# Kernel tuning notes

Hardware: AMD Instinct MI355X
Metric: run time of the kernel (lower is better)

## Reference

```python
import jax, jax.numpy as jnp
import numpy as np

B, S, T, C, HS = 32, 8, 512, 128, 128


def setup_inputs() -> dict:
    key = jax.random.key(0)
    k1, k2, k3, k4, k5 = jax.random.split(key, 5)
    x = jax.random.normal(k1, (B, T, C), dtype=jnp.float32)
    adjacent = jax.random.uniform(k2, (B, S, T, T), dtype=jnp.float32)
    scale = 1.0 / np.sqrt(C)
    Wq = jax.random.normal(k3, (C, HS), dtype=jnp.float32) * scale
    Wk = jax.random.normal(k4, (C, HS), dtype=jnp.float32) * scale
    Wv = jax.random.normal(k5, (C, HS), dtype=jnp.float32) * scale
    return {"x": x, "adjacent": adjacent, "Wq": Wq, "Wk": Wk, "Wv": Wv}


def reference(x, adjacent, Wq, Wk, Wv):
    # x: [B,T,C], adjacent: [B,S,T,T]
    Cdim = x.shape[-1]
    q = x @ Wq            # [B,T,HS]
    k = x @ Wk            # [B,T,HS]
    v = x @ Wv            # [B,T,HS]
    # scaled scores (note: original scales by C^-0.5, not head_size^-0.5)
    wei = jnp.einsum('btd,bud->btu', q, k) * (Cdim ** -0.5)  # [B,T,T]
    # multiplicative adjacency mask, broadcast over S
    wei = wei[:, None, :, :] * adjacent                       # [B,S,T,T]
    wei = jax.nn.softmax(wei, axis=-1)
    # dropout p=0.0 -> identity
    out = jnp.einsum('bstu,bud->bstd', wei, v)                # [B,S,T,HS]
    return out
```

## Files before the change

### kernel.cpp

```cpp
#include <hip/hip_runtime.h>
#include <hip/hip_bf16.h>
#include <stdint.h>

#define NB 32
#define NS 8
#define NT 512
#define NC 128
#define NH 128

typedef __bf16 bf16_t;
typedef bf16_t bf16x8 __attribute__((ext_vector_type(8)));
typedef bf16_t bf16x4 __attribute__((ext_vector_type(4)));
typedef float  f32x4  __attribute__((ext_vector_type(4)));

__global__ __launch_bounds__(256) void k_split(const float* __restrict__ in,
                                               bf16_t* __restrict__ hi,
                                               bf16_t* __restrict__ lo, int n4) {
  int i = blockIdx.x * 256 + threadIdx.x;
  if (i >= n4) return;
  f32x4 x = ((const f32x4*)in)[i];
  bf16x4 h, l;
#pragma unroll
  for (int j = 0; j < 4; j++) {
    bf16_t hb = (bf16_t)x[j];
    h[j] = hb;
    l[j] = (bf16_t)(x[j] - (float)hb);
  }
  ((bf16x4*)hi)[i] = h;
  ((bf16x4*)lo)[i] = l;
}

__global__ void k_prep_w(const float* __restrict__ Wq, const float* __restrict__ Wk,
                         const float* __restrict__ Wv, bf16_t* __restrict__ Wth,
                         bf16_t* __restrict__ Wtl) {
  int w = blockIdx.x >> 7;
  int h = blockIdx.x & 127;
  int c = threadIdx.x;
  const float* W = (w == 0) ? Wq : (w == 1) ? Wk : Wv;
  float x = W[c * NH + h];
  bf16_t hb = (bf16_t)x;
  int o = (w * 128 + h) * 128 + c;
  Wth[o] = hb;
  Wtl[o] = (bf16_t)(x - (float)hb);
}

__global__ __launch_bounds__(256) void k_qkv(const bf16_t* __restrict__ xh,
                                             const bf16_t* __restrict__ xl,
                                             const bf16_t* __restrict__ Wth,
                                             const bf16_t* __restrict__ Wtl,
                                             bf16_t* __restrict__ qh,
                                             bf16_t* __restrict__ ql,
                                             bf16_t* __restrict__ kh,
                                             bf16_t* __restrict__ kl,
                                             bf16_t* __restrict__ vt) {
  int mat = blockIdx.y;
  int t0 = blockIdx.x * 64;
  int lane = threadIdx.x & 63;
  int wave = threadIdx.x >> 6;
  int l15 = lane & 15;
  int kq = (lane >> 4) * 8;
  int row = t0 + wave * 16 + l15;
  const bf16_t* Wh = Wth + mat * NC * NH;
  const bf16_t* Wl = Wtl + mat * NC * NH;

  f32x4 zero = {0.f, 0.f, 0.f, 0.f};
  f32x4 acc[8];
#pragma unroll
  for (int i = 0; i < 8; i++) acc[i] = zero;

#pragma unroll
  for (int k0 = 0; k0 < NC; k0 += 32) {
    bf16x8 ah = *(const bf16x8*)(xh + (size_t)row * NC + k0 + kq);
    bf16x8 al = *(const bf16x8*)(xl + (size_t)row * NC + k0 + kq);
#pragma unroll
    for (int nt = 0; nt < 8; nt++) {
      bf16x8 bh = *(const bf16x8*)(Wh + (nt * 16 + l15) * NC + k0 + kq);
      bf16x8 bl = *(const bf16x8*)(Wl + (nt * 16 + l15) * NC + k0 + kq);
      acc[nt] = __builtin_amdgcn_mfma_f32_16x16x32_bf16(ah, bh, acc[nt], 0, 0, 0);
      acc[nt] = __builtin_amdgcn_mfma_f32_16x16x32_bf16(ah, bl, acc[nt], 0, 0, 0);
      acc[nt] = __builtin_amdgcn_mfma_f32_16x16x32_bf16(al, bh, acc[nt], 0, 0, 0);
    }
  }

  int trow = t0 + wave * 16 + (lane >> 4) * 4;
  if (mat < 2) {
    bf16_t* dh = (mat == 0) ? qh : kh;
    bf16_t* dl = (mat == 0) ? ql : kl;
#pragma unroll
    for (int nt = 0; nt < 8; nt++) {
      int h = nt * 16 + l15;
#pragma unroll
      for (int r = 0; r < 4; r++) {
        float v = acc[nt][r];
        bf16_t hb = (bf16_t)v;
        dh[(size_t)(trow + r) * NH + h] = hb;
        dl[(size_t)(trow + r) * NH + h] = (bf16_t)(v - (float)hb);
      }
    }
  } else {
    int b = trow >> 9;
    int tl = trow & 511;
#pragma unroll
    for (int nt = 0; nt < 8; nt++) {
      int h = nt * 16 + l15;
      bf16x4 pk;
#pragma unroll
      for (int r = 0; r < 4; r++) pk[r] = (bf16_t)acc[nt][r];
      *(bf16x4*)(vt + ((size_t)b * NH + h) * NT + tl) = pk;
    }
  }
}

__global__ __launch_bounds__(256) void k_scores(const bf16_t* __restrict__ qh,
                                                const bf16_t* __restrict__ ql,
                                                const bf16_t* __restrict__ kh,
                                                const bf16_t* __restrict__ kl,
                                                float* __restrict__ wei) {
  int b = blockIdx.y;
  int mt = blockIdx.x >> 3;
  int ut = blockIdx.x & 7;
  int lane = threadIdx.x & 63;
  int wave = threadIdx.x >> 6;
  int l15 = lane & 15;
  int kq = (lane >> 4) * 8;
  int m0 = mt * 64 + wave * 16;
  int u0 = ut * 64;
  const float scale = 0.08838834764831845f;

  f32x4 zero = {0.f, 0.f, 0.f, 0.f};
  f32x4 acc[4];
#pragma unroll
  for (int i = 0; i < 4; i++) acc[i] = zero;

  size_t qbase = ((size_t)b * NT + m0 + l15) * NH;
  size_t kbase = ((size_t)b * NT + u0 + l15) * NH;

#pragma unroll
  for (int k0 = 0; k0 < NH; k0 += 32) {
    bf16x8 ah = *(const bf16x8*)(qh + qbase + k0 + kq);
    bf16x8 al = *(const bf16x8*)(ql + qbase + k0 + kq);
#pragma unroll
    for (int nt = 0; nt < 4; nt++) {
      bf16x8 bh = *(const bf16x8*)(kh + kbase + (size_t)nt * 16 * NH + k0 + kq);
      bf16x8 bl = *(const bf16x8*)(kl + kbase + (size_t)nt * 16 * NH + k0 + kq);
      acc[nt] = __builtin_amdgcn_mfma_f32_16x16x32_bf16(ah, bh, acc[nt], 0, 0, 0);
      acc[nt] = __builtin_amdgcn_mfma_f32_16x16x32_bf16(ah, bl, acc[nt], 0, 0, 0);
      acc[nt] = __builtin_amdgcn_mfma_f32_16x16x32_bf16(al, bh, acc[nt], 0, 0, 0);
    }
  }

  int t = m0 + (lane >> 4) * 4;
#pragma unroll
  for (int nt = 0; nt < 4; nt++) {
    int u = u0 + nt * 16 + l15;
#pragma unroll
    for (int r = 0; r < 4; r++)
      wei[((size_t)b * NT + t + r) * NT + u] = acc[nt][r] * scale;
  }
}

#define PLD 520

__global__ __launch_bounds__(256) void k_attn(const float* __restrict__ wei,
                                              const float* __restrict__ adj,
                                              const bf16_t* __restrict__ vt,
                                              float* __restrict__ out) {
  __shared__ bf16_t p[32 * PLD];
  int t0 = blockIdx.x * 32;
  int s = blockIdx.y;
  int b = blockIdx.z;
  int lane = threadIdx.x & 63;
  int wave = threadIdx.x >> 6;

#pragma unroll
  for (int rr = 0; rr < 8; rr++) {
    int r = wave * 8 + rr;
    const float* wrow = wei + ((size_t)b * NT + t0 + r) * NT;
    const float* arow = adj + (((size_t)b * NS + s) * NT + t0 + r) * NT;
    f32x4 w0 = ((const f32x4*)wrow)[lane];
    f32x4 w1 = ((const f32x4*)wrow)[64 + lane];
    f32x4 a0 = ((const f32x4*)arow)[lane];
    f32x4 a1 = ((const f32x4*)arow)[64 + lane];
    bf16x4 e0, e1;
#pragma unroll
    for (int j = 0; j < 4; j++) e0[j] = (bf16_t)__expf(w0[j] * a0[j]);
#pragma unroll
    for (int j = 0; j < 4; j++) e1[j] = (bf16_t)__expf(w1[j] * a1[j]);
    *(bf16x4*)&p[r * PLD + lane * 4] = e0;
    *(bf16x4*)&p[r * PLD + 256 + lane * 4] = e1;
  }
  __syncthreads();

  int l15 = lane & 15;
  int kq = (lane >> 4) * 8;
  int m0 = (wave & 1) * 16;
  int h0 = (wave >> 1) * 64;
  f32x4 zero = {0.f, 0.f, 0.f, 0.f};
  f32x4 acc[4];
#pragma unroll
  for (int i = 0; i < 4; i++) acc[i] = zero;
  f32x4 accl = zero;
  bf16x8 ones;
#pragma unroll
  for (int j = 0; j < 8; j++) ones[j] = (bf16_t)1.0f;
  const bf16_t* vb = vt + (size_t)b * NH * NT;

#pragma unroll 4
  for (int k0 = 0; k0 < NT; k0 += 32) {
    bf16x8 a = *(const bf16x8*)&p[(m0 + l15) * PLD + k0 + kq];
    accl = __builtin_amdgcn_mfma_f32_16x16x32_bf16(a, ones, accl, 0, 0, 0);
#pragma unroll
    for (int nt = 0; nt < 4; nt++) {
      bf16x8 bfr = *(const bf16x8*)(vb + (size_t)(h0 + nt * 16 + l15) * NT + k0 + kq);
      acc[nt] = __builtin_amdgcn_mfma_f32_16x16x32_bf16(a, bfr, acc[nt], 0, 0, 0);
    }
  }

  int tl = m0 + (lane >> 4) * 4;
  float linv[4];
#pragma unroll
  for (int r = 0; r < 4; r++) linv[r] = 1.0f / accl[r];
  float* obase = out + (((size_t)b * NS + s) * NT + t0) * NH;
#pragma unroll
  for (int nt = 0; nt < 4; nt++) {
    int h = h0 + nt * 16 + l15;
#pragma unroll
    for (int r = 0; r < 4; r++)
      obase[(size_t)(tl + r) * NH + h] = acc[nt][r] * linv[r];
  }
}

extern "C" void kernel_launch(void* const* d_in, const int* in_sizes, int n_in,
                              void* d_out, int out_size, void* d_ws, size_t ws_size,
                              hipStream_t stream) {
  const float* x = (const float*)d_in[0];
  const float* adj = (const float*)d_in[1];
  const float* Wq = (const float*)d_in[2];
  const float* Wk = (const float*)d_in[3];
  const float* Wv = (const float*)d_in[4];
  float* out = (float*)d_out;

  const size_t BTC = (size_t)NB * NT * NC;

  char* base = (char*)d_ws;
  bf16_t* xh = (bf16_t*)base;  base += BTC * 2;
  bf16_t* xl = (bf16_t*)base;  base += BTC * 2;
  bf16_t* Wth = (bf16_t*)base; base += (size_t)3 * NC * NH * 2;
  bf16_t* Wtl = (bf16_t*)base; base += (size_t)3 * NC * NH * 2;
  bf16_t* qh = (bf16_t*)base;  base += BTC * 2;
  bf16_t* ql = (bf16_t*)base;  base += BTC * 2;
  bf16_t* kh = (bf16_t*)base;  base += BTC * 2;
  bf16_t* kl = (bf16_t*)base;  base += BTC * 2;
  bf16_t* vt = (bf16_t*)base;  base += BTC * 2;
  float* wei = (float*)base;   base += (size_t)NB * NT * NT * 4;
  (void)in_sizes; (void)n_in; (void)out_size; (void)ws_size;

  k_split<<<(int)(BTC / 4 / 256), 256, 0, stream>>>(x, xh, xl, (int)(BTC / 4));
  k_prep_w<<<384, 128, 0, stream>>>(Wq, Wk, Wv, Wth, Wtl);
  k_qkv<<<dim3((int)(NB * NT / 64), 3), 256, 0, stream>>>(xh, xl, Wth, Wtl,
                                                          qh, ql, kh, kl, vt);
  k_scores<<<dim3(64, NB), 256, 0, stream>>>(qh, ql, kh, kl, wei);
  k_attn<<<dim3(NT / 32, NS, NB), 256, 0, stream>>>(wei, adj, vt, out);
}
```

Before: 535.3 us.

## Loop over S inside attention block with double-buffered P and adj prefetch

The attention kernel now handles a 16-row tile for all 8 S slices inside one block. The wei rows are loaded once per block and reused across S instead of being reloaded per slice. The adj rows for the next slice are prefetched into registers while the current slice's MFMA loop runs, and a double-buffered shared P tile lets compute overlap with writing the next exponentials. The trade-off is a smaller grid (1024 blocks) with a serial S loop, 16-row MFMA tiles that reuse V less per load, and higher register pressure under the launch_bounds(256,4) hint.

```diff
diff --git a/kernel.cpp b/kernel.cpp
--- a/kernel.cpp
+++ b/kernel.cpp
@@ -161,72 +161,92 @@
 
 #define PLD 520
 
-__global__ __launch_bounds__(256) void k_attn(const float* __restrict__ wei,
-                                              const float* __restrict__ adj,
-                                              const bf16_t* __restrict__ vt,
-                                              float* __restrict__ out) {
-  __shared__ bf16_t p[32 * PLD];
-  int t0 = blockIdx.x * 32;
-  int s = blockIdx.y;
-  int b = blockIdx.z;
+__global__ __launch_bounds__(256, 4) void k_attn(const float* __restrict__ wei,
+                                                 const float* __restrict__ adj,
+                                                 const bf16_t* __restrict__ vt,
+                                                 float* __restrict__ out) {
+  __shared__ bf16_t p[2][16 * PLD];
+  int t0 = blockIdx.x * 16;
+  int b = blockIdx.y;
   int lane = threadIdx.x & 63;
   int wave = threadIdx.x >> 6;
-
-#pragma unroll
-  for (int rr = 0; rr < 8; rr++) {
-    int r = wave * 8 + rr;
-    const float* wrow = wei + ((size_t)b * NT + t0 + r) * NT;
-    const float* arow = adj + (((size_t)b * NS + s) * NT + t0 + r) * NT;
-    f32x4 w0 = ((const f32x4*)wrow)[lane];
-    f32x4 w1 = ((const f32x4*)wrow)[64 + lane];
-    f32x4 a0 = ((const f32x4*)arow)[lane];
-    f32x4 a1 = ((const f32x4*)arow)[64 + lane];
-    bf16x4 e0, e1;
-#pragma unroll
-    for (int j = 0; j < 4; j++) e0[j] = (bf16_t)__expf(w0[j] * a0[j]);
-#pragma unroll
-    for (int j = 0; j < 4; j++) e1[j] = (bf16_t)__expf(w1[j] * a1[j]);
-    *(bf16x4*)&p[r * PLD + lane * 4] = e0;
-    *(bf16x4*)&p[r * PLD + 256 + lane * 4] = e1;
-  }
-  __syncthreads();
-
   int l15 = lane & 15;
   int kq = (lane >> 4) * 8;
-  int m0 = (wave & 1) * 16;
-  int h0 = (wave >> 1) * 64;
-  f32x4 zero = {0.f, 0.f, 0.f, 0.f};
-  f32x4 acc[4];
-#pragma unroll
-  for (int i = 0; i < 4; i++) acc[i] = zero;
-  f32x4 accl = zero;
+  int h0 = wave * 32;
+
+  f32x4 wf0[4], wf1[4];
+#pragma unroll
+  for (int rr = 0; rr < 4; rr++) {
+    const float* wrow = wei + ((size_t)b * NT + t0 + wave * 4 + rr) * NT;
+    wf0[rr] = ((const f32x4*)wrow)[lane];
+    wf1[rr] = ((const f32x4*)wrow)[64 + lane];
+  }
+
+  const bf16_t* vb = vt + (size_t)b * NH * NT;
   bf16x8 ones;
 #pragma unroll
   for (int j = 0; j < 8; j++) ones[j] = (bf16_t)1.0f;
-  const bf16_t* vb = vt + (size_t)b * NH * NT;
-
+
+  f32x4 a0[4], a1[4];
+#pragma unroll
+  for (int rr = 0; rr < 4; rr++) {
+    const float* arow = adj + ((size_t)b * NS * NT + t0 + wave * 4 + rr) * NT;
+    a0[rr] = ((const f32x4*)arow)[lane];
+    a1[rr] = ((const f32x4*)arow)[64 + lane];
+  }
+
+  for (int s = 0; s < NS; s++) {
+    bf16_t* pb = &p[s & 1][0];
+#pragma unroll
+    for (int rr = 0; rr < 4; rr++) {
+      int r = wave * 4 + rr;
+      bf16x4 e0, e1;
+#pragma unroll
+      for (int j = 0; j < 4; j++) e0[j] = (bf16_t)__expf(wf0[rr][j] * a0[rr][j]);
+#pragma unroll
+      for (int j = 0; j < 4; j++) e1[j] = (bf16_t)__expf(wf1[rr][j] * a1[rr][j]);
+      *(bf16x4*)&pb[r * PLD + lane * 4] = e0;
+      *(bf16x4*)&pb[r * PLD + 256 + lane * 4] = e1;
+    }
+    __syncthreads();
+
+    if (s + 1 < NS) {
+#pragma unroll
+      for (int rr = 0; rr < 4; rr++) {
+        const float* arow =
+            adj + (((size_t)b * NS + s + 1) * NT + t0 + wave * 4 + rr) * NT;
+        a0[rr] = ((const f32x4*)arow)[lane];
+        a1[rr] = ((const f32x4*)arow)[64 + lane];
+      }
+    }
+
+    f32x4 zero = {0.f, 0.f, 0.f, 0.f};
+    f32x4 acc[2] = {zero, zero};
+    f32x4 accl = zero;
 #pragma unroll 4
-  for (int k0 = 0; k0 < NT; k0 += 32) {
-    bf16x8 a = *(const bf16x8*)&p[(m0 + l15) * PLD + k0 + kq];
-    accl = __builtin_amdgcn_mfma_f32_16x16x32_bf16(a, ones, accl, 0, 0, 0);
-#pragma unroll
-    for (int nt = 0; nt < 4; nt++) {
-      bf16x8 bfr = *(const bf16x8*)(vb + (size_t)(h0 + nt * 16 + l15) * NT + k0 + kq);
-      acc[nt] = __builtin_amdgcn_mfma_f32_16x16x32_bf16(a, bfr, acc[nt], 0, 0, 0);
-    }
-  }
-
-  int tl = m0 + (lane >> 4) * 4;
-  float linv[4];
-#pragma unroll
-  for (int r = 0; r < 4; r++) linv[r] = 1.0f / accl[r];
-  float* obase = out + (((size_t)b * NS + s) * NT + t0) * NH;
-#pragma unroll
-  for (int nt = 0; nt < 4; nt++) {
-    int h = h0 + nt * 16 + l15;
-#pragma unroll
-    for (int r = 0; r < 4; r++)
-      obase[(size_t)(tl + r) * NH + h] = acc[nt][r] * linv[r];
+    for (int k0 = 0; k0 < NT; k0 += 32) {
+      bf16x8 afr = *(const bf16x8*)&pb[l15 * PLD + k0 + kq];
+      accl = __builtin_amdgcn_mfma_f32_16x16x32_bf16(afr, ones, accl, 0, 0, 0);
+#pragma unroll
+      for (int nt = 0; nt < 2; nt++) {
+        bf16x8 bfr =
+            *(const bf16x8*)(vb + (size_t)(h0 + nt * 16 + l15) * NT + k0 + kq);
+        acc[nt] = __builtin_amdgcn_mfma_f32_16x16x32_bf16(afr, bfr, acc[nt], 0, 0, 0);
+      }
+    }
+
+    int tl = (lane >> 4) * 4;
+    float linv[4];
+#pragma unroll
+    for (int r = 0; r < 4; r++) linv[r] = 1.0f / accl[r];
+    float* obase = out + (((size_t)b * NS + s) * NT + t0) * NH;
+#pragma unroll
+    for (int nt = 0; nt < 2; nt++) {
+      int h = h0 + nt * 16 + l15;
+#pragma unroll
+      for (int r = 0; r < 4; r++)
+        obase[(size_t)(tl + r) * NH + h] = acc[nt][r] * linv[r];
+    }
   }
 }
 
@@ -260,5 +280,5 @@
   k_qkv<<<dim3((int)(NB * NT / 64), 3), 256, 0, stream>>>(xh, xl, Wth, Wtl,
                                                           qh, ql, kh, kl, vt);
   k_scores<<<dim3(64, NB), 256, 0, stream>>>(qh, ql, kh, kl, wei);
-  k_attn<<<dim3(NT / 32, NS, NB), 256, 0, stream>>>(wei, adj, vt, out);
-}
+  k_attn<<<dim3(NT / 16, NB), 256, 0, stream>>>(wei, adj, vt, out);
+}
```

After: 534.2 us. About the same (-0.2%).

## Fuse score computation into attention kernel and fold scale into Wq

Applied to the files above, without the earlier changes.

Removes the separate scores kernel and the fp32 wei buffer in global memory. Each 512-thread block computes its 16-row score tile once with split-bf16 MFMA, then loops over all 8 S slices, applying the adjacency mask, exp and the PV product with a double-buffered LDS tile. The C^-0.5 scale is folded into Wq during weight prep. This saves writing and re-reading wei eight times, at the cost of smaller per-block tiles, adjacency loads of one float per lane, and serial S iterations inside each block.

```diff
diff --git a/kernel.cpp b/kernel.cpp
--- a/kernel.cpp
+++ b/kernel.cpp
@@ -38,6 +38,7 @@
   int c = threadIdx.x;
   const float* W = (w == 0) ? Wq : (w == 1) ? Wk : Wv;
   float x = W[c * NH + h];
+  if (w == 0) x *= 0.08838834764831845f;
   bf16_t hb = (bf16_t)x;
   int o = (w * 128 + h) * 128 + c;
   Wth[o] = hb;
@@ -111,122 +112,83 @@
   }
 }
 
-__global__ __launch_bounds__(256) void k_scores(const bf16_t* __restrict__ qh,
-                                                const bf16_t* __restrict__ ql,
-                                                const bf16_t* __restrict__ kh,
-                                                const bf16_t* __restrict__ kl,
-                                                float* __restrict__ wei) {
+#define PLD 520
+
+__global__ __launch_bounds__(512, 8) void k_attn(const bf16_t* __restrict__ qh,
+                                                 const bf16_t* __restrict__ ql,
+                                                 const bf16_t* __restrict__ kh,
+                                                 const bf16_t* __restrict__ kl,
+                                                 const float* __restrict__ adj,
+                                                 const bf16_t* __restrict__ vt,
+                                                 float* __restrict__ out) {
+  __shared__ bf16_t p[2][16 * PLD];
+  int t0 = blockIdx.x * 16;
   int b = blockIdx.y;
-  int mt = blockIdx.x >> 3;
-  int ut = blockIdx.x & 7;
   int lane = threadIdx.x & 63;
   int wave = threadIdx.x >> 6;
   int l15 = lane & 15;
-  int kq = (lane >> 4) * 8;
-  int m0 = mt * 64 + wave * 16;
-  int u0 = ut * 64;
-  const float scale = 0.08838834764831845f;
+  int q4 = lane >> 4;
+  int kq = q4 * 8;
+  int u0 = wave * 64;
+  int h0 = wave * 16;
 
   f32x4 zero = {0.f, 0.f, 0.f, 0.f};
-  f32x4 acc[4];
-#pragma unroll
-  for (int i = 0; i < 4; i++) acc[i] = zero;
-
-  size_t qbase = ((size_t)b * NT + m0 + l15) * NH;
-  size_t kbase = ((size_t)b * NT + u0 + l15) * NH;
-
-#pragma unroll
-  for (int k0 = 0; k0 < NH; k0 += 32) {
-    bf16x8 ah = *(const bf16x8*)(qh + qbase + k0 + kq);
-    bf16x8 al = *(const bf16x8*)(ql + qbase + k0 + kq);
+  f32x4 wacc[4];
+#pragma unroll
+  for (int i = 0; i < 4; i++) wacc[i] = zero;
+  {
+    size_t qb = ((size_t)b * NT + t0 + l15) * NH;
+    size_t kb = ((size_t)b * NT + u0 + l15) * NH;
+#pragma unroll
+    for (int k0 = 0; k0 < NH; k0 += 32) {
+      bf16x8 ah = *(const bf16x8*)(qh + qb + k0 + kq);
+      bf16x8 al = *(const bf16x8*)(ql + qb + k0 + kq);
+#pragma unroll
+      for (int nt = 0; nt < 4; nt++) {
+        bf16x8 bh = *(const bf16x8*)(kh + kb + (size_t)nt * 16 * NH + k0 + kq);
+        bf16x8 bl = *(const bf16x8*)(kl + kb + (size_t)nt * 16 * NH + k0 + kq);
+        wacc[nt] = __builtin_amdgcn_mfma_f32_16x16x32_bf16(ah, bh, wacc[nt], 0, 0, 0);
+        wacc[nt] = __builtin_amdgcn_mfma_f32_16x16x32_bf16(ah, bl, wacc[nt], 0, 0, 0);
+        wacc[nt] = __builtin_amdgcn_mfma_f32_16x16x32_bf16(al, bh, wacc[nt], 0, 0, 0);
+      }
+    }
+  }
+
+  const bf16_t* vb = vt + (size_t)b * NH * NT;
+  bf16x8 ones;
+#pragma unroll
+  for (int j = 0; j < 8; j++) ones[j] = (bf16_t)1.0f;
+
+  for (int s = 0; s < NS; s++) {
+    bf16_t* pb = &p[s & 1][0];
+    const float* abase =
+        adj + (((size_t)b * NS + s) * NT + t0 + q4 * 4) * NT + u0 + l15;
 #pragma unroll
     for (int nt = 0; nt < 4; nt++) {
-      bf16x8 bh = *(const bf16x8*)(kh + kbase + (size_t)nt * 16 * NH + k0 + kq);
-      bf16x8 bl = *(const bf16x8*)(kl + kbase + (size_t)nt * 16 * NH + k0 + kq);
-      acc[nt] = __builtin_amdgcn_mfma_f32_16x16x32_bf16(ah, bh, acc[nt], 0, 0, 0);
-      acc[nt] = __builtin_amdgcn_mfma_f32_16x16x32_bf16(ah, bl, acc[nt], 0, 0, 0);
-      acc[nt] = __builtin_amdgcn_mfma_f32_16x16x32_bf16(al, bh, acc[nt], 0, 0, 0);
-    }
-  }
-
-  int t = m0 + (lane >> 4) * 4;
-#pragma unroll
-  for (int nt = 0; nt < 4; nt++) {
-    int u = u0 + nt * 16 + l15;
-#pragma unroll
-    for (int r = 0; r < 4; r++)
-      wei[((size_t)b * NT + t + r) * NT + u] = acc[nt][r] * scale;
-  }
-}
-
-#define PLD 520
-
-__global__ __launch_bounds__(256) void k_attn(const float* __restrict__ wei,
-                                              const float* __restrict__ adj,
-                                              const bf16_t* __restrict__ vt,
-                                              float* __restrict__ out) {
-  __shared__ bf16_t p[32 * PLD];
-  int t0 = blockIdx.x * 32;
-  int s = blockIdx.y;
-  int b = blockIdx.z;
-  int lane = threadIdx.x & 63;
-  int wave = threadIdx.x >> 6;
-
-#pragma unroll
-  for (int rr = 0; rr < 8; rr++) {
-    int r = wave * 8 + rr;
-    const float* wrow = wei + ((size_t)b * NT + t0 + r) * NT;
-    const float* arow = adj + (((size_t)b * NS + s) * NT + t0 + r) * NT;
-    f32x4 w0 = ((const f32x4*)wrow)[lane];
-    f32x4 w1 = ((const f32x4*)wrow)[64 + lane];
-    f32x4 a0 = ((const f32x4*)arow)[lane];
-    f32x4 a1 = ((const f32x4*)arow)[64 + lane];
-    bf16x4 e0, e1;
-#pragma unroll
-    for (int j = 0; j < 4; j++) e0[j] = (bf16_t)__expf(w0[j] * a0[j]);
-#pragma unroll
-    for (int j = 0; j < 4; j++) e1[j] = (bf16_t)__expf(w1[j] * a1[j]);
-    *(bf16x4*)&p[r * PLD + lane * 4] = e0;
-    *(bf16x4*)&p[r * PLD + 256 + lane * 4] = e1;
-  }
-  __syncthreads();
-
-  int l15 = lane & 15;
-  int kq = (lane >> 4) * 8;
-  int m0 = (wave & 1) * 16;
-  int h0 = (wave >> 1) * 64;
-  f32x4 zero = {0.f, 0.f, 0.f, 0.f};
-  f32x4 acc[4];
-#pragma unroll
-  for (int i = 0; i < 4; i++) acc[i] = zero;
-  f32x4 accl = zero;
-  bf16x8 ones;
-#pragma unroll
-  for (int j = 0; j < 8; j++) ones[j] = (bf16_t)1.0f;
-  const bf16_t* vb = vt + (size_t)b * NH * NT;
-
+#pragma unroll
+      for (int r = 0; r < 4; r++) {
+        float a = abase[(size_t)r * NT + nt * 16];
+        float e = __expf(wacc[nt][r] * a);
+        pb[(q4 * 4 + r) * PLD + u0 + nt * 16 + l15] = (bf16_t)e;
+      }
+    }
+    __syncthreads();
+
+    f32x4 acc = zero, accl = zero;
 #pragma unroll 4
-  for (int k0 = 0; k0 < NT; k0 += 32) {
-    bf16x8 a = *(const bf16x8*)&p[(m0 + l15) * PLD + k0 + kq];
-    accl = __builtin_amdgcn_mfma_f32_16x16x32_bf16(a, ones, accl, 0, 0, 0);
-#pragma unroll
-    for (int nt = 0; nt < 4; nt++) {
-      bf16x8 bfr = *(const bf16x8*)(vb + (size_t)(h0 + nt * 16 + l15) * NT + k0 + kq);
-      acc[nt] = __builtin_amdgcn_mfma_f32_16x16x32_bf16(a, bfr, acc[nt], 0, 0, 0);
-    }
-  }
-
-  int tl = m0 + (lane >> 4) * 4;
-  float linv[4];
-#pragma unroll
-  for (int r = 0; r < 4; r++) linv[r] = 1.0f / accl[r];
-  float* obase = out + (((size_t)b * NS + s) * NT + t0) * NH;
-#pragma unroll
-  for (int nt = 0; nt < 4; nt++) {
-    int h = h0 + nt * 16 + l15;
-#pragma unroll
-    for (int r = 0; r < 4; r++)
-      obase[(size_t)(tl + r) * NH + h] = acc[nt][r] * linv[r];
+    for (int k0 = 0; k0 < NT; k0 += 32) {
+      bf16x8 afr = *(const bf16x8*)&pb[l15 * PLD + k0 + kq];
+      accl = __builtin_amdgcn_mfma_f32_16x16x32_bf16(afr, ones, accl, 0, 0, 0);
+      bf16x8 bfr = *(const bf16x8*)(vb + (size_t)(h0 + l15) * NT + k0 + kq);
+      acc = __builtin_amdgcn_mfma_f32_16x16x32_bf16(afr, bfr, acc, 0, 0, 0);
+    }
+
+    float* obase = out + (((size_t)b * NS + s) * NT + t0) * NH;
+#pragma unroll
+    for (int r = 0; r < 4; r++) {
+      float linv = 1.0f / accl[r];
+      obase[(size_t)(q4 * 4 + r) * NH + h0 + l15] = acc[r] * linv;
+    }
   }
 }
 
@@ -252,13 +214,11 @@
   bf16_t* kh = (bf16_t*)base;  base += BTC * 2;
   bf16_t* kl = (bf16_t*)base;  base += BTC * 2;
   bf16_t* vt = (bf16_t*)base;  base += BTC * 2;
-  float* wei = (float*)base;   base += (size_t)NB * NT * NT * 4;
   (void)in_sizes; (void)n_in; (void)out_size; (void)ws_size;
 
   k_split<<<(int)(BTC / 4 / 256), 256, 0, stream>>>(x, xh, xl, (int)(BTC / 4));
   k_prep_w<<<384, 128, 0, stream>>>(Wq, Wk, Wv, Wth, Wtl);
   k_qkv<<<dim3((int)(NB * NT / 64), 3), 256, 0, stream>>>(xh, xl, Wth, Wtl,
                                                           qh, ql, kh, kl, vt);
-  k_scores<<<dim3(64, NB), 256, 0, stream>>>(qh, ql, kh, kl, wei);
-  k_attn<<<dim3(NT / 32, NS, NB), 256, 0, stream>>>(wei, adj, vt, out);
-}
+  k_attn<<<dim3(NT / 16, NB), 512, 0, stream>>>(qh, ql, kh, kl, adj, vt, out);
+}
```

After: 537.1 us. No clear change (+0.3%).
